# Kernel optimization log

Measured on AMD Instinct MI355X. Metric: run time of the kernel, lower is better.

Reference implementation:

```python
import jax, jax.numpy as jnp
import numpy as np

ALPHA = 1.702   # GLU sigmoid scale
LIMIT = 7.0     # clamp limit
K = 2           # experts per token


def setup_inputs() -> dict:
    key = jax.random.key(0)
    ks = jax.random.split(key, 4)
    B, S, H, E, I = 1, 1024, 1024, 8, 1024
    return {
        "hidden_states": jax.random.normal(ks[0], (B, S, H), jnp.float32),
        "router_weight": jax.random.normal(ks[1], (E, H), jnp.float32),
        "router_bias": jnp.zeros((E,), jnp.float32),
        "gate_up_proj": jax.random.normal(ks[2], (E, H, 2 * I), jnp.float32) * 0.02,
        "gate_up_bias": jnp.zeros((E, 2 * I), jnp.float32),
        "down_proj": jax.random.normal(ks[3], (E, I, H), jnp.float32) * 0.02,
        "down_bias": jnp.zeros((E, H), jnp.float32),
    }


def reference(hidden_states, router_weight, router_bias, gate_up_proj,
              gate_up_bias, down_proj, down_bias):
    B, S, H = hidden_states.shape
    E = router_weight.shape[0]
    I = down_proj.shape[1]
    T = B * S

    flat = hidden_states.reshape(T, H)

    # Router: softmax over experts, top-K selection (weights NOT renormalized).
    logits = flat @ router_weight.T + router_bias               # [T, E]
    scores = jax.nn.softmax(logits, axis=-1)
    topk_vals, topk_idx = jax.lax.top_k(scores, K)              # [T, K]

    # Dense per-token expert weight matrix (equivalent of dispatch metadata +
    # combine * topk_weights in the tt pipeline); top-k indices are unique.
    w = jnp.zeros((T, E), scores.dtype).at[
        jnp.arange(T)[:, None], topk_idx].set(topk_vals)        # [T, E]

    # Expert MLP with clamped GLU (gpt-oss style).
    gu = jnp.einsum('th,ehf->tef', flat, gate_up_proj) + gate_up_bias  # [T,E,2I]
    gate = jnp.minimum(gu[..., :I], LIMIT)
    up = jnp.clip(gu[..., I:], -LIMIT, LIMIT)
    glu = gate * jax.nn.sigmoid(gate * ALPHA)
    act = (up + 1.0) * glu                                       # [T, E, I]

    down = jnp.einsum('tei,eih->teh', act, down_proj) + down_bias  # [T, E, H]

    # Weighted combine over selected experts.
    out = jnp.einsum('teh,te->th', down, w)
    return out.reshape(B, S, H)
```

## Files before the change

kernel.cpp:

```cpp
#include <hip/hip_runtime.h>
#include <hip/hip_bf16.h>


typedef unsigned short u16;
typedef __attribute__((ext_vector_type(8))) __bf16 bf16x8;
typedef __attribute__((ext_vector_type(4))) float f32x4;

#define T_TOK 1024
#define H_DIM 1024
#define E_NUM 8
#define I_DIM 1024
#define ALPHA 1.702f
#define LIMIT 7.0f
#define LSTR 72
#define AROWS 2176

__device__ __forceinline__ u16 f2bf(float f) {
    unsigned u = __builtin_bit_cast(unsigned, f);
    u = (u + 0x7FFFu + ((u >> 16) & 1u)) >> 16;
    return (u16)u;
}

__device__ __forceinline__ unsigned pk2(float lo, float hi) {
#if defined(__has_builtin) && __has_builtin(__builtin_amdgcn_cvt_pk_bf16_f32)
    typedef __attribute__((ext_vector_type(2))) __bf16 bf16x2_t;
    bf16x2_t v = __builtin_amdgcn_cvt_pk_bf16_f32(lo, hi);
    return __builtin_bit_cast(unsigned, v);
#else
    return (unsigned)f2bf(lo) | ((unsigned)f2bf(hi) << 16);
#endif
}

__device__ __forceinline__ f32x4 mfma16(bf16x8 a, bf16x8 b, f32x4 c) {
    return __builtin_amdgcn_mfma_f32_16x16x32_bf16(a, b, c, 0, 0, 0);
}

__device__ __forceinline__ void expert_range(const int* counts, int e,
                                             int& cnt, int& abase) {
    int a = 0, c = 0;
#pragma unroll
    for (int i = 0; i < E_NUM; ++i) {
        int v = counts[i];
        if (i < e) a += v;
        if (i == e) c = v;
    }
    cnt = c; abase = a;
}

__global__ __launch_bounds__(256) void k_router(
    const float* __restrict__ x, const float* __restrict__ rw,
    const float* __restrict__ rb, const float* __restrict__ db,
    int* __restrict__ counts, int* __restrict__ tok_list,
    float* __restrict__ w_list, u16* __restrict__ xb,
    float* __restrict__ out)
{
    const int t = blockIdx.x;
    const int tid = threadIdx.x;
    const float4 xv = *(const float4*)(x + (size_t)t * H_DIM + tid * 4);

    *(uint2*)(xb + (size_t)t * H_DIM + tid * 4) =
        make_uint2(pk2(xv.x, xv.y), pk2(xv.z, xv.w));

    float p[E_NUM];
#pragma unroll
    for (int e = 0; e < E_NUM; ++e) {
        const float4 wv = *(const float4*)(rw + e * H_DIM + tid * 4);
        p[e] = xv.x * wv.x + xv.y * wv.y + xv.z * wv.z + xv.w * wv.w;
    }
#pragma unroll
    for (int off = 32; off; off >>= 1) {
#pragma unroll
        for (int e = 0; e < E_NUM; ++e) p[e] += __shfl_down(p[e], off, 64);
    }
    __shared__ float red[4][E_NUM];
    __shared__ int se[2];
    __shared__ float sw[2];
    const int lane = tid & 63, wvid = tid >> 6;
    if (lane == 0) {
#pragma unroll
        for (int e = 0; e < E_NUM; ++e) red[wvid][e] = p[e];
    }
    __syncthreads();
    if (tid == 0) {
        float lg[E_NUM];
#pragma unroll
        for (int e = 0; e < E_NUM; ++e)
            lg[e] = red[0][e] + red[1][e] + red[2][e] + red[3][e] + rb[e];
        float m1 = -1e30f, m2 = -1e30f; int i1 = 0, i2 = 0;
#pragma unroll
        for (int e = 0; e < E_NUM; ++e) {
            float l = lg[e];
            if (l > m1) { m2 = m1; i2 = i1; m1 = l; i1 = e; }
            else if (l > m2) { m2 = l; i2 = e; }
        }
        float s = 0.f;
#pragma unroll
        for (int e = 0; e < E_NUM; ++e) s += __expf(lg[e] - m1);
        const float w0 = 1.0f / s;
        const float w1 = __expf(m2 - m1) / s;
        int slot0 = atomicAdd(&counts[i1], 1);
        tok_list[i1 * T_TOK + slot0] = t;
        w_list[i1 * T_TOK + slot0] = w0;
        int slot1 = atomicAdd(&counts[i2], 1);
        tok_list[i2 * T_TOK + slot1] = t;
        w_list[i2 * T_TOK + slot1] = w1;
        se[0] = i1; se[1] = i2; sw[0] = w0; sw[1] = w1;
    }
    __syncthreads();
    const int e0 = se[0], e1 = se[1];
    const float w0 = sw[0], w1 = sw[1];
    const int c = tid * 4;
    float4 d0 = *(const float4*)(db + e0 * H_DIM + c);
    float4 d1 = *(const float4*)(db + e1 * H_DIM + c);
    float4 o;
    o.x = w0 * d0.x + w1 * d1.x;
    o.y = w0 * d0.y + w1 * d1.y;
    o.z = w0 * d0.z + w1 * d1.z;
    o.w = w0 * d0.w + w1 * d1.w;
    *(float4*)(out + (size_t)t * H_DIM + c) = o;
}

__global__ __launch_bounds__(256) void k_prep(
    const float* __restrict__ gup, const float* __restrict__ dp,
    u16* __restrict__ gup_t, u16* __restrict__ dp_t)
{
    __shared__ unsigned Lt[64 * 36];
    const int bid = blockIdx.x;
    const float* src; u16* dst; int C, ct, kt;
    if (bid < 4096) {
        int e = bid >> 9, t = bid & 511;
        ct = t & 31; kt = t >> 5; C = 2048;
        src = gup + ((size_t)e << 21);
        dst = gup_t + ((size_t)e << 21);
    } else {
        int b2 = bid - 4096;
        int e = b2 >> 8, t = b2 & 255;
        ct = t & 15; kt = t >> 4; C = 1024;
        src = dp + ((size_t)e << 20);
        dst = dp_t + ((size_t)e << 20);
    }
    const int k0 = kt * 64, c0 = ct * 64;
    const int tid = threadIdx.x;

    const int kp = tid >> 3, q = tid & 7;
    const float* s0 = src + (size_t)(k0 + 2 * kp) * C + c0 + q * 8;
    float4 r0a = *(const float4*)(s0);
    float4 r0b = *(const float4*)(s0 + 4);
    float4 r1a = *(const float4*)(s0 + C);
    float4 r1b = *(const float4*)(s0 + C + 4);
    const float* e0 = (const float*)&r0a;
    const float* e1 = (const float*)&r0b;
    const float* f0 = (const float*)&r1a;
    const float* f1 = (const float*)&r1b;
#pragma unroll
    for (int j = 0; j < 8; ++j) {
        float lo = (j < 4) ? e0[j] : e1[j - 4];
        float hi = (j < 4) ? f0[j] : f1[j - 4];
        int cl = q * 8 + j;
        int grp = (kp >> 2) ^ q;
        Lt[cl * 36 + (grp << 2) + (kp & 3)] = pk2(lo, hi);
    }
    __syncthreads();

    const int cl = tid >> 2, ko2 = tid & 3;
#pragma unroll
    for (int i = 0; i < 2; ++i) {
        int koct = ko2 * 2 + i;
        int grp = koct ^ (cl >> 3);
        uint4 v = *(const uint4*)&Lt[cl * 36 + (grp << 2)];
        *(uint4*)(dst + (size_t)(c0 + cl) * 1024 + k0 + koct * 8) = v;
    }
}

__global__ __launch_bounds__(256) void k_gateup(
    const u16* __restrict__ gup_t, const float* __restrict__ gub,
    const int* __restrict__ counts, const int* __restrict__ tok_list,
    const u16* __restrict__ xb, u16* __restrict__ act)
{
    const int e = blockIdx.z;
    int cnt, abase;
    expert_range(counts, e, cnt, abase);
    const int m0 = blockIdx.y * 128;
    if (m0 >= cnt) return;
    const int n0 = blockIdx.x * 32;
    const int tid = threadIdx.x;

    __shared__ __align__(16) u16 As[2][128 * LSTR];
    __shared__ __align__(16) u16 Bs[2][64 * LSTR];

    const int arow_i = tid >> 1, akh = (tid & 1) * 32;
    const int aslot = m0 + arow_i;
    const int atok = (aslot < cnt) ? tok_list[e * T_TOK + aslot] : 0;
    const u16* asrc = xb + (size_t)atok * H_DIM + akh;
    const int aoff = arow_i * LSTR + akh;

    const int cl = tid >> 3, koct = tid & 7;
    const u16* bgs = gup_t + ((size_t)(e * 2048 + n0 + cl)) * 1024 + koct * 8;
    const u16* bus = bgs + (size_t)1024 * 1024;
    const int boffg = cl * LSTR + koct * 8;
    const int boffu = (32 + cl) * LSTR + koct * 8;

    const int lane = tid & 63, wv = tid >> 6;
    const int fm = lane & 15, kg = lane >> 4;

    f32x4 accg[2][2], accu[2][2];
#pragma unroll
    for (int mt = 0; mt < 2; ++mt)
#pragma unroll
        for (int nt = 0; nt < 2; ++nt) {
            accg[mt][nt] = (f32x4){0.f, 0.f, 0.f, 0.f};
            accu[mt][nt] = (f32x4){0.f, 0.f, 0.f, 0.f};
        }

#define GU_LOAD(A0, A1, A2, A3, G, U, CH)                                      \
    {                                                                          \
        const u16* ap_ = asrc + (CH) * 64;                                     \
        A0 = *(const uint4*)(ap_);                                             \
        A1 = *(const uint4*)(ap_ + 8);                                         \
        A2 = *(const uint4*)(ap_ + 16);                                        \
        A3 = *(const uint4*)(ap_ + 24);                                        \
        G = *(const uint4*)(bgs + (CH) * 64);                                  \
        U = *(const uint4*)(bus + (CH) * 64);                                  \
    }
#define GU_STORE(BUF, A0, A1, A2, A3, G, U)                                    \
    {                                                                          \
        *(uint4*)&As[BUF][aoff]      = A0;                                     \
        *(uint4*)&As[BUF][aoff + 8]  = A1;                                     \
        *(uint4*)&As[BUF][aoff + 16] = A2;                                     \
        *(uint4*)&As[BUF][aoff + 24] = A3;                                     \
        *(uint4*)&Bs[BUF][boffg] = G;                                          \
        *(uint4*)&Bs[BUF][boffu] = U;                                          \
    }
#define GU_MFMA(BUF)                                                           \
    {                                                                          \
        _Pragma("unroll")                                                      \
        for (int sub = 0; sub < 2; ++sub) {                                    \
            _Pragma("unroll")                                                  \
            for (int mt = 0; mt < 2; ++mt) {                                   \
                bf16x8 af = *(const bf16x8*)&As[BUF][(wv * 32 + mt * 16 + fm) * LSTR + sub * 32 + kg * 8]; \
                _Pragma("unroll")                                              \
                for (int nt = 0; nt < 2; ++nt) {                               \
                    bf16x8 bg = *(const bf16x8*)&Bs[BUF][(nt * 16 + fm) * LSTR + sub * 32 + kg * 8]; \
                    bf16x8 bu = *(const bf16x8*)&Bs[BUF][(32 + nt * 16 + fm) * LSTR + sub * 32 + kg * 8]; \
                    accg[mt][nt] = mfma16(af, bg, accg[mt][nt]);               \
                    accu[mt][nt] = mfma16(af, bu, accu[mt][nt]);               \
                }                                                              \
            }                                                                  \
        }                                                                      \
    }

    uint4 A0r0, A1r0, A2r0, A3r0, Gr0, Ur0;
    uint4 A0r1, A1r1, A2r1, A3r1, Gr1, Ur1;
    GU_LOAD(A0r0, A1r0, A2r0, A3r0, Gr0, Ur0, 0);
    GU_LOAD(A0r1, A1r1, A2r1, A3r1, Gr1, Ur1, 1);
    GU_STORE(0, A0r0, A1r0, A2r0, A3r0, Gr0, Ur0);
    GU_LOAD(A0r0, A1r0, A2r0, A3r0, Gr0, Ur0, 2);

#pragma unroll 4
    for (int i = 0; i < 16; ++i) {
        __syncthreads();
        const int b = i & 1;
        if (i < 15) {
            if (b == 0) { GU_STORE(1, A0r1, A1r1, A2r1, A3r1, Gr1, Ur1); }
            else        { GU_STORE(0, A0r0, A1r0, A2r0, A3r0, Gr0, Ur0); }
        }
        if (i < 13) {
            if (b == 0) { GU_LOAD(A0r1, A1r1, A2r1, A3r1, Gr1, Ur1, i + 3); }
            else        { GU_LOAD(A0r0, A1r0, A2r0, A3r0, Gr0, Ur0, i + 3); }
        }
        GU_MFMA(b);
    }
#undef GU_LOAD
#undef GU_STORE
#undef GU_MFMA

#pragma unroll
    for (int mt = 0; mt < 2; ++mt) {
#pragma unroll
        for (int r = 0; r < 4; ++r) {
            int rowb = wv * 32 + mt * 16 + kg * 4 + r;
            int slot = m0 + rowb;
            if (slot >= cnt) continue;
            size_t arow_o = (size_t)(abase + slot) * I_DIM;
#pragma unroll
            for (int nt = 0; nt < 2; ++nt) {
                int cn = n0 + nt * 16 + fm;
                float g = accg[mt][nt][r] + gub[e * 2048 + cn];
                float u = accu[mt][nt][r] + gub[e * 2048 + 1024 + cn];
                g = fminf(g, LIMIT);
                u = fminf(fmaxf(u, -LIMIT), LIMIT);
                float glu = g / (1.f + __expf(-ALPHA * g));
                act[arow_o + cn] = f2bf((u + 1.f) * glu);
            }
        }
    }
}

__global__ __launch_bounds__(256) void k_down(
    const u16* __restrict__ dp_t,
    const int* __restrict__ counts, const int* __restrict__ tok_list,
    const float* __restrict__ w_list,
    const u16* __restrict__ act, float* __restrict__ out)
{
    const int e = blockIdx.z & 7, ks = blockIdx.z >> 3;
    int cnt, abase;
    expert_range(counts, e, cnt, abase);
    const int m0 = blockIdx.y * 128;
    if (m0 >= cnt) return;
    const int n0 = blockIdx.x * 64;
    const int tid = threadIdx.x;

    __shared__ __align__(16) u16 As[2][128 * LSTR];
    __shared__ __align__(16) u16 Bs[2][64 * LSTR];

    const int arow_i = tid >> 1, akh = (tid & 1) * 32;
    const u16* asrc = act + (size_t)(abase + m0 + arow_i) * I_DIM + ks * 512 + akh;
    const int aoff = arow_i * LSTR + akh;

    const int cl = tid >> 3, koct = tid & 7;
    const u16* bs0 = dp_t + ((size_t)(e * 1024 + n0 + cl)) * 1024 + ks * 512 + koct * 8;
    const u16* bs1 = bs0 + (size_t)32 * 1024;
    const int boff0 = cl * LSTR + koct * 8;
    const int boff1 = (32 + cl) * LSTR + koct * 8;

    const int lane = tid & 63, wv = tid >> 6;
    const int fm = lane & 15, kg = lane >> 4;

    f32x4 acc[2][4];
#pragma unroll
    for (int mt = 0; mt < 2; ++mt)
#pragma unroll
        for (int nt = 0; nt < 4; ++nt) acc[mt][nt] = (f32x4){0.f, 0.f, 0.f, 0.f};

#define DN_LOAD(A0, A1, A2, A3, B0, B1, CH)                                    \
    {                                                                          \
        const u16* ap_ = asrc + (CH) * 64;                                     \
        A0 = *(const uint4*)(ap_);                                             \
        A1 = *(const uint4*)(ap_ + 8);                                         \
        A2 = *(const uint4*)(ap_ + 16);                                        \
        A3 = *(const uint4*)(ap_ + 24);                                        \
        B0 = *(const uint4*)(bs0 + (CH) * 64);                                 \
        B1 = *(const uint4*)(bs1 + (CH) * 64);                                 \
    }
#define DN_STORE(BUF, A0, A1, A2, A3, B0, B1)                                  \
    {                                                                          \
        *(uint4*)&As[BUF][aoff]      = A0;                                     \
        *(uint4*)&As[BUF][aoff + 8]  = A1;                                     \
        *(uint4*)&As[BUF][aoff + 16] = A2;                                     \
        *(uint4*)&As[BUF][aoff + 24] = A3;                                     \
        *(uint4*)&Bs[BUF][boff0] = B0;                                         \
        *(uint4*)&Bs[BUF][boff1] = B1;                                         \
    }
#define DN_MFMA(BUF)                                                           \
    {                                                                          \
        _Pragma("unroll")                                                      \
        for (int sub = 0; sub < 2; ++sub) {                                    \
            _Pragma("unroll")                                                  \
            for (int mt = 0; mt < 2; ++mt) {                                   \
                bf16x8 af = *(const bf16x8*)&As[BUF][(wv * 32 + mt * 16 + fm) * LSTR + sub * 32 + kg * 8]; \
                _Pragma("unroll")                                              \
                for (int nt = 0; nt < 4; ++nt) {                               \
                    bf16x8 bb = *(const bf16x8*)&Bs[BUF][(nt * 16 + fm) * LSTR + sub * 32 + kg * 8]; \
                    acc[mt][nt] = mfma16(af, bb, acc[mt][nt]);                 \
                }                                                              \
            }                                                                  \
        }                                                                      \
    }

    uint4 A0r0, A1r0, A2r0, A3r0, B0r0, B1r0;
    uint4 A0r1, A1r1, A2r1, A3r1, B0r1, B1r1;
    DN_LOAD(A0r0, A1r0, A2r0, A3r0, B0r0, B1r0, 0);
    DN_LOAD(A0r1, A1r1, A2r1, A3r1, B0r1, B1r1, 1);
    DN_STORE(0, A0r0, A1r0, A2r0, A3r0, B0r0, B1r0);
    DN_LOAD(A0r0, A1r0, A2r0, A3r0, B0r0, B1r0, 2);

#pragma unroll 4
    for (int i = 0; i < 8; ++i) {
        __syncthreads();
        const int b = i & 1;
        if (i < 7) {
            if (b == 0) { DN_STORE(1, A0r1, A1r1, A2r1, A3r1, B0r1, B1r1); }
            else        { DN_STORE(0, A0r0, A1r0, A2r0, A3r0, B0r0, B1r0); }
        }
        if (i < 5) {
            if (b == 0) { DN_LOAD(A0r1, A1r1, A2r1, A3r1, B0r1, B1r1, i + 3); }
            else        { DN_LOAD(A0r0, A1r0, A2r0, A3r0, B0r0, B1r0, i + 3); }
        }
        DN_MFMA(b);
    }
#undef DN_LOAD
#undef DN_STORE
#undef DN_MFMA

#pragma unroll
    for (int mt = 0; mt < 2; ++mt) {
#pragma unroll
        for (int r = 0; r < 4; ++r) {
            int rowb = wv * 32 + mt * 16 + kg * 4 + r;
            int slot = m0 + rowb;
            if (slot >= cnt) continue;
            float wgt = w_list[e * T_TOK + slot];
            int tok = tok_list[e * T_TOK + slot];
            float* orow = out + (size_t)tok * H_DIM + n0;
#pragma unroll
            for (int nt = 0; nt < 4; ++nt)
                atomicAdd(orow + nt * 16 + fm, acc[mt][nt][r] * wgt);
        }
    }
}

extern "C" void kernel_launch(void* const* d_in, const int* in_sizes, int n_in,
                              void* d_out, int out_size, void* d_ws, size_t ws_size,
                              hipStream_t stream) {
    const float* x   = (const float*)d_in[0];
    const float* rw  = (const float*)d_in[1];
    const float* rb  = (const float*)d_in[2];
    const float* gup = (const float*)d_in[3];
    const float* gub = (const float*)d_in[4];
    const float* dp  = (const float*)d_in[5];
    const float* db  = (const float*)d_in[6];
    float* out = (float*)d_out;

    char* ws = (char*)d_ws;
    int*   counts   = (int*)(ws);
    int*   tok_list = (int*)(ws + 64);
    float* w_list   = (float*)(ws + 32832);
    u16*   xb       = (u16*)(ws + 65600);
    u16*   gup_t    = (u16*)(ws + 2162752);
    u16*   dp_t     = (u16*)(ws + 35717184);
    u16*   act      = (u16*)(ws + 52494400);

    hipMemsetAsync(counts, 0, 64, stream);
    k_router<<<T_TOK, 256, 0, stream>>>(x, rw, rb, db, counts, tok_list, w_list,
                                        xb, out);
    k_prep<<<6144, 256, 0, stream>>>(gup, dp, gup_t, dp_t);
    k_gateup<<<dim3(32, 8, 8), 256, 0, stream>>>(gup_t, gub, counts, tok_list,
                                                 xb, act);
    k_down<<<dim3(16, 8, 16), 256, 0, stream>>>(dp_t, counts, tok_list, w_list,
                                                act, out);
}
```

Before: 234.6 us.

## Fuse router and weight-transpose prep kernels; batch four tiles per prep block

Merges the router kernel and the weight conversion/transpose kernel into one launch. The first 1024 blocks do routing and the remaining 1536 blocks do the transposes. Each prep block now handles four 64x64 column tiles instead of one, double-buffering its global loads across tiles to overlap memory latency. This removes one kernel launch and cuts the block count, at the cost of extra barriers and more registers per thread.

New measurement: 235.2 us. No clear change (+0.2%).

```diff
diff --git a/kernel.cpp b/kernel.cpp
--- a/kernel.cpp
+++ b/kernel.cpp
@@ -47,129 +47,157 @@
     cnt = c; abase = a;
 }
 
-__global__ __launch_bounds__(256) void k_router(
+__global__ __launch_bounds__(256) void k_fused_rp(
     const float* __restrict__ x, const float* __restrict__ rw,
     const float* __restrict__ rb, const float* __restrict__ db,
     int* __restrict__ counts, int* __restrict__ tok_list,
-    float* __restrict__ w_list, u16* __restrict__ xb,
-    float* __restrict__ out)
+    float* __restrict__ w_list, u16* __restrict__ xb, float* __restrict__ out,
+    const float* __restrict__ gup, const float* __restrict__ dp,
+    u16* __restrict__ gup_t, u16* __restrict__ dp_t)
 {
-    const int t = blockIdx.x;
-    const int tid = threadIdx.x;
-    const float4 xv = *(const float4*)(x + (size_t)t * H_DIM + tid * 4);
-
-    *(uint2*)(xb + (size_t)t * H_DIM + tid * 4) =
-        make_uint2(pk2(xv.x, xv.y), pk2(xv.z, xv.w));
-
-    float p[E_NUM];
-#pragma unroll
-    for (int e = 0; e < E_NUM; ++e) {
-        const float4 wv = *(const float4*)(rw + e * H_DIM + tid * 4);
-        p[e] = xv.x * wv.x + xv.y * wv.y + xv.z * wv.z + xv.w * wv.w;
-    }
-#pragma unroll
-    for (int off = 32; off; off >>= 1) {
-#pragma unroll
-        for (int e = 0; e < E_NUM; ++e) p[e] += __shfl_down(p[e], off, 64);
-    }
     __shared__ float red[4][E_NUM];
     __shared__ int se[2];
     __shared__ float sw[2];
-    const int lane = tid & 63, wvid = tid >> 6;
-    if (lane == 0) {
-#pragma unroll
-        for (int e = 0; e < E_NUM; ++e) red[wvid][e] = p[e];
-    }
-    __syncthreads();
-    if (tid == 0) {
-        float lg[E_NUM];
-#pragma unroll
-        for (int e = 0; e < E_NUM; ++e)
-            lg[e] = red[0][e] + red[1][e] + red[2][e] + red[3][e] + rb[e];
-        float m1 = -1e30f, m2 = -1e30f; int i1 = 0, i2 = 0;
+    __shared__ unsigned Lt[64 * 36];
+    const int tid = threadIdx.x;
+
+    if (blockIdx.x < 1024) {
+        const int t = blockIdx.x;
+        const float4 xv = *(const float4*)(x + (size_t)t * H_DIM + tid * 4);
+
+        *(uint2*)(xb + (size_t)t * H_DIM + tid * 4) =
+            make_uint2(pk2(xv.x, xv.y), pk2(xv.z, xv.w));
+
+        float p[E_NUM];
 #pragma unroll
         for (int e = 0; e < E_NUM; ++e) {
-            float l = lg[e];
-            if (l > m1) { m2 = m1; i2 = i1; m1 = l; i1 = e; }
-            else if (l > m2) { m2 = l; i2 = e; }
-        }
-        float s = 0.f;
-#pragma unroll
-        for (int e = 0; e < E_NUM; ++e) s += __expf(lg[e] - m1);
-        const float w0 = 1.0f / s;
-        const float w1 = __expf(m2 - m1) / s;
-        int slot0 = atomicAdd(&counts[i1], 1);
-        tok_list[i1 * T_TOK + slot0] = t;
-        w_list[i1 * T_TOK + slot0] = w0;
-        int slot1 = atomicAdd(&counts[i2], 1);
-        tok_list[i2 * T_TOK + slot1] = t;
-        w_list[i2 * T_TOK + slot1] = w1;
-        se[0] = i1; se[1] = i2; sw[0] = w0; sw[1] = w1;
-    }
-    __syncthreads();
-    const int e0 = se[0], e1 = se[1];
-    const float w0 = sw[0], w1 = sw[1];
-    const int c = tid * 4;
-    float4 d0 = *(const float4*)(db + e0 * H_DIM + c);
-    float4 d1 = *(const float4*)(db + e1 * H_DIM + c);
-    float4 o;
-    o.x = w0 * d0.x + w1 * d1.x;
-    o.y = w0 * d0.y + w1 * d1.y;
-    o.z = w0 * d0.z + w1 * d1.z;
-    o.w = w0 * d0.w + w1 * d1.w;
-    *(float4*)(out + (size_t)t * H_DIM + c) = o;
-}
-
-__global__ __launch_bounds__(256) void k_prep(
-    const float* __restrict__ gup, const float* __restrict__ dp,
-    u16* __restrict__ gup_t, u16* __restrict__ dp_t)
-{
-    __shared__ unsigned Lt[64 * 36];
-    const int bid = blockIdx.x;
-    const float* src; u16* dst; int C, ct, kt;
-    if (bid < 4096) {
-        int e = bid >> 9, t = bid & 511;
-        ct = t & 31; kt = t >> 5; C = 2048;
-        src = gup + ((size_t)e << 21);
-        dst = gup_t + ((size_t)e << 21);
+            const float4 wv = *(const float4*)(rw + e * H_DIM + tid * 4);
+            p[e] = xv.x * wv.x + xv.y * wv.y + xv.z * wv.z + xv.w * wv.w;
+        }
+#pragma unroll
+        for (int off = 32; off; off >>= 1) {
+#pragma unroll
+            for (int e = 0; e < E_NUM; ++e) p[e] += __shfl_down(p[e], off, 64);
+        }
+        const int lane = tid & 63, wvid = tid >> 6;
+        if (lane == 0) {
+#pragma unroll
+            for (int e = 0; e < E_NUM; ++e) red[wvid][e] = p[e];
+        }
+        __syncthreads();
+        if (tid == 0) {
+            float lg[E_NUM];
+#pragma unroll
+            for (int e = 0; e < E_NUM; ++e)
+                lg[e] = red[0][e] + red[1][e] + red[2][e] + red[3][e] + rb[e];
+            float m1 = -1e30f, m2 = -1e30f; int i1 = 0, i2 = 0;
+#pragma unroll
+            for (int e = 0; e < E_NUM; ++e) {
+                float l = lg[e];
+                if (l > m1) { m2 = m1; i2 = i1; m1 = l; i1 = e; }
+                else if (l > m2) { m2 = l; i2 = e; }
+            }
+            float s = 0.f;
+#pragma unroll
+            for (int e = 0; e < E_NUM; ++e) s += __expf(lg[e] - m1);
+            const float w0 = 1.0f / s;
+            const float w1 = __expf(m2 - m1) / s;
+            int slot0 = atomicAdd(&counts[i1], 1);
+            tok_list[i1 * T_TOK + slot0] = t;
+            w_list[i1 * T_TOK + slot0] = w0;
+            int slot1 = atomicAdd(&counts[i2], 1);
+            tok_list[i2 * T_TOK + slot1] = t;
+            w_list[i2 * T_TOK + slot1] = w1;
+            se[0] = i1; se[1] = i2; sw[0] = w0; sw[1] = w1;
+        }
+        __syncthreads();
+        const int e0 = se[0], e1 = se[1];
+        const float w0 = sw[0], w1 = sw[1];
+        const int c = tid * 4;
+        float4 d0 = *(const float4*)(db + e0 * H_DIM + c);
+        float4 d1 = *(const float4*)(db + e1 * H_DIM + c);
+        float4 o;
+        o.x = w0 * d0.x + w1 * d1.x;
+        o.y = w0 * d0.y + w1 * d1.y;
+        o.z = w0 * d0.z + w1 * d1.z;
+        o.w = w0 * d0.w + w1 * d1.w;
+        *(float4*)(out + (size_t)t * H_DIM + c) = o;
+        return;
+    }
+
+    const int bid = blockIdx.x - 1024;
+    const float* src; u16* dst; int C, kt, ctb;
+    if (bid < 1024) {
+        int e = bid >> 7, g = bid & 127;
+        kt = g >> 3; ctb = (g & 7) * 4; C = 2048;
+        src = gup + ((size_t)e << 21); dst = gup_t + ((size_t)e << 21);
     } else {
-        int b2 = bid - 4096;
-        int e = b2 >> 8, t = b2 & 255;
-        ct = t & 15; kt = t >> 4; C = 1024;
-        src = dp + ((size_t)e << 20);
-        dst = dp_t + ((size_t)e << 20);
-    }
-    const int k0 = kt * 64, c0 = ct * 64;
-    const int tid = threadIdx.x;
-
+        int b2 = bid - 1024;
+        int e = b2 >> 6, g = b2 & 63;
+        kt = g >> 2; ctb = (g & 3) * 4; C = 1024;
+        src = dp + ((size_t)e << 20); dst = dp_t + ((size_t)e << 20);
+    }
+    const int k0 = kt * 64;
     const int kp = tid >> 3, q = tid & 7;
-    const float* s0 = src + (size_t)(k0 + 2 * kp) * C + c0 + q * 8;
-    float4 r0a = *(const float4*)(s0);
-    float4 r0b = *(const float4*)(s0 + 4);
-    float4 r1a = *(const float4*)(s0 + C);
-    float4 r1b = *(const float4*)(s0 + C + 4);
-    const float* e0 = (const float*)&r0a;
-    const float* e1 = (const float*)&r0b;
-    const float* f0 = (const float*)&r1a;
-    const float* f1 = (const float*)&r1b;
-#pragma unroll
-    for (int j = 0; j < 8; ++j) {
-        float lo = (j < 4) ? e0[j] : e1[j - 4];
-        float hi = (j < 4) ? f0[j] : f1[j - 4];
-        int cl = q * 8 + j;
-        int grp = (kp >> 2) ^ q;
-        Lt[cl * 36 + (grp << 2) + (kp & 3)] = pk2(lo, hi);
-    }
-    __syncthreads();
-
     const int cl = tid >> 2, ko2 = tid & 3;
-#pragma unroll
-    for (int i = 0; i < 2; ++i) {
-        int koct = ko2 * 2 + i;
-        int grp = koct ^ (cl >> 3);
-        uint4 v = *(const uint4*)&Lt[cl * 36 + (grp << 2)];
-        *(uint4*)(dst + (size_t)(c0 + cl) * 1024 + k0 + koct * 8) = v;
-    }
+    const float* sbase = src + (size_t)(k0 + 2 * kp) * C + q * 8;
+
+#define P_LOAD(RA, RB, RC, RD, I)                                              \
+    {                                                                          \
+        const float* s_ = sbase + (ctb + (I)) * 64;                            \
+        RA = *(const float4*)(s_);                                             \
+        RB = *(const float4*)(s_ + 4);                                         \
+        RC = *(const float4*)(s_ + C);                                         \
+        RD = *(const float4*)(s_ + C + 4);                                     \
+    }
+#define P_LDSW(RA, RB, RC, RD)                                                 \
+    {                                                                          \
+        const float* e0_ = (const float*)&RA; const float* e1_ = (const float*)&RB; \
+        const float* f0_ = (const float*)&RC; const float* f1_ = (const float*)&RD; \
+        _Pragma("unroll")                                                      \
+        for (int j = 0; j < 8; ++j) {                                          \
+            float lo_ = (j < 4) ? e0_[j] : e1_[j - 4];                         \
+            float hi_ = (j < 4) ? f0_[j] : f1_[j - 4];                         \
+            int c_ = q * 8 + j;                                                \
+            int grp_ = (kp >> 2) ^ q;                                          \
+            Lt[c_ * 36 + (grp_ << 2) + (kp & 3)] = pk2(lo_, hi_);              \
+        }                                                                      \
+    }
+#define P_OUT(I)                                                               \
+    {                                                                          \
+        const int c0_ = (ctb + (I)) * 64;                                      \
+        _Pragma("unroll")                                                      \
+        for (int i2 = 0; i2 < 2; ++i2) {                                       \
+            int koct_ = ko2 * 2 + i2;                                          \
+            int grp_ = koct_ ^ (cl >> 3);                                      \
+            uint4 v_ = *(const uint4*)&Lt[cl * 36 + (grp_ << 2)];              \
+            *(uint4*)(dst + (size_t)(c0_ + cl) * 1024 + k0 + koct_ * 8) = v_;  \
+        }                                                                      \
+    }
+
+    float4 Aa, Ab, Ac, Ad, Ba, Bb, Bc, Bd;
+    P_LOAD(Aa, Ab, Ac, Ad, 0);
+    P_LOAD(Ba, Bb, Bc, Bd, 1);
+    P_LDSW(Aa, Ab, Ac, Ad);
+    __syncthreads();
+    P_OUT(0);
+    P_LOAD(Aa, Ab, Ac, Ad, 2);
+    __syncthreads();
+    P_LDSW(Ba, Bb, Bc, Bd);
+    __syncthreads();
+    P_OUT(1);
+    P_LOAD(Ba, Bb, Bc, Bd, 3);
+    __syncthreads();
+    P_LDSW(Aa, Ab, Ac, Ad);
+    __syncthreads();
+    P_OUT(2);
+    __syncthreads();
+    P_LDSW(Ba, Bb, Bc, Bd);
+    __syncthreads();
+    P_OUT(3);
+#undef P_LOAD
+#undef P_LDSW
+#undef P_OUT
 }
 
 __global__ __launch_bounds__(256) void k_gateup(
@@ -431,9 +459,8 @@
     u16*   act      = (u16*)(ws + 52494400);
 
     hipMemsetAsync(counts, 0, 64, stream);
-    k_router<<<T_TOK, 256, 0, stream>>>(x, rw, rb, db, counts, tok_list, w_list,
-                                        xb, out);
-    k_prep<<<6144, 256, 0, stream>>>(gup, dp, gup_t, dp_t);
+    k_fused_rp<<<2560, 256, 0, stream>>>(x, rw, rb, db, counts, tok_list,
+                                         w_list, xb, out, gup, dp, gup_t, dp_t);
     k_gateup<<<dim3(32, 8, 8), 256, 0, stream>>>(gup_t, gub, counts, tok_list,
                                                  xb, act);
     k_down<<<dim3(16, 8, 16), 256, 0, stream>>>(dp_t, counts, tok_list, w_list,
```
